# Performance work log

Hardware: AMD Instinct MI355X
Metric: run time of the kernel (lower is better)

The kernel has to match this reference:

```python
import jax, jax.numpy as jnp
import numpy as np

HEADS = 8
MEM_LEN = 32


def _mha(q, k, v, Wq, bq, Wk, bk, Wv, bv, Wo, bo):
    # torch nn.MultiheadAttention, batch_first=False. q: [Lq,B,E], k/v: [Lk,B,E]
    Lq, B, E = q.shape
    d = E // HEADS

    def proj(t, W, b):
        p = t @ W.T + b
        return p.reshape(t.shape[0], B, HEADS, d).transpose(1, 2, 0, 3)  # [B,h,L,d]

    qh, kh, vh = proj(q, Wq, bq), proj(k, Wk, bk), proj(v, Wv, bv)
    scale = 1.0 / jnp.sqrt(jnp.asarray(d, q.dtype))
    att = jax.nn.softmax(jnp.einsum('bhqd,bhkd->bhqk', qh * scale, kh), axis=-1)
    out = jnp.einsum('bhqk,bhkd->bhqd', att, vh)          # [B,h,Lq,d]
    out = out.transpose(2, 0, 1, 3).reshape(Lq, B, E)
    return out @ Wo.T + bo


def _forward(x, h, c, memK, memV, externalK, externalV,
             W_ih, W_hh, b_ih, b_hh,
             sWq, sbq, sWk, sbk, sWv, sbv, sWo, sbo,
             cWq, cbq, cWk, cbk, cWv, cbv, cWo, cbo,
             Wres, bres, Wrout, brout, Wcomp, bcomp, Wexp, bexp, Wgate, bgate):
    H = h.shape[1]
    # LSTMCell (torch gate order i, f, g, o)
    gates = x @ W_ih.T + b_ih + h @ W_hh.T + b_hh
    i, f, g, o = jnp.split(gates, 4, axis=1)
    c_next = jax.nn.sigmoid(f) * c + jax.nn.sigmoid(i) * jnp.tanh(g)
    h_lstm = jax.nn.sigmoid(o) * jnp.tanh(c_next)
    # append detached h_lstm to short memory, keep last MEM_LEN entries
    cur = jax.lax.stop_gradient(h_lstm)[None]                      # [1,B,H]
    memK_new = jnp.concatenate([memK, cur], axis=0)[-MEM_LEN:]     # [ML,B,H]
    memV_new = jnp.concatenate([memV, cur], axis=0)[-MEM_LEN:]
    qSelf = h_lstm[None]                                           # [1,B,H]
    self_out = _mha(qSelf, memK_new, memV_new, sWq, sbq, sWk, sbk, sWv, sbv, sWo, sbo)[0]
    ext_out = _mha(qSelf, externalK, externalV, cWq, cbq, cWk, cbk, cWv, cbv, cWo, cbo)[0]
    rw = jax.nn.softmax(h_lstm @ Wrout.T + brout, axis=1)          # [B,2] router
    routed_attn = rw[:, :1] * self_out + rw[:, 1:2] * ext_out
    routed = h_lstm + routed_attn + routed_attn @ Wres.T + bres
    temporal_summary = memK_new.mean(axis=0)                       # [B,H]
    compressed = temporal_summary @ Wcomp.T + bcomp                # [B,H//4]
    expanded = compressed @ Wexp.T + bexp                          # [B,H]
    reps = -(-H // compressed.shape[1])
    compressed_expanded = jnp.tile(compressed, (1, reps))[:, :H]
    gate = jax.nn.sigmoid(jnp.concatenate([x, routed], axis=1) @ Wgate.T + bgate)
    hCT = compressed_expanded + gate * (expanded - compressed_expanded)  # torch.lerp
    hFinal = (h_lstm + routed + hCT) / 3.0                         # dropout = identity (eval)
    return hFinal, h_lstm, c_next


def setup_inputs() -> dict:
    key = jax.random.key(0)
    ks = jax.random.split(key, 34)
    B, I, H, ML, EL = 2048, 1024, 1024, 32, 32
    BN = H // 4
    rn = lambda k, s, sc=1.0: jax.random.normal(k, s, dtype=jnp.float32) * sc
    return {
        'x': rn(ks[0], (B, I)), 'h': rn(ks[1], (B, H)), 'c': rn(ks[2], (B, H)),
        'memK': rn(ks[3], (ML, B, H)), 'memV': rn(ks[4], (ML, B, H)),
        'externalK': rn(ks[5], (EL, B, H)), 'externalV': rn(ks[6], (EL, B, H)),
        'W_ih': rn(ks[7], (4 * H, I), 0.02), 'W_hh': rn(ks[8], (4 * H, H), 0.02),
        'b_ih': jnp.zeros((4 * H,), jnp.float32), 'b_hh': jnp.zeros((4 * H,), jnp.float32),
        'sWq': rn(ks[9], (H, H), 0.02), 'sbq': rn(ks[10], (H,), 0.02),
        'sWk': rn(ks[11], (H, H), 0.02), 'sbk': rn(ks[12], (H,), 0.02),
        'sWv': rn(ks[13], (H, H), 0.02), 'sbv': rn(ks[14], (H,), 0.02),
        'sWo': rn(ks[15], (H, H), 0.02), 'sbo': rn(ks[16], (H,), 0.02),
        'cWq': rn(ks[17], (H, H), 0.02), 'cbq': rn(ks[18], (H,), 0.02),
        'cWk': rn(ks[19], (H, H), 0.02), 'cbk': rn(ks[20], (H,), 0.02),
        'cWv': rn(ks[21], (H, H), 0.02), 'cbv': rn(ks[22], (H,), 0.02),
        'cWo': rn(ks[23], (H, H), 0.02), 'cbo': rn(ks[24], (H,), 0.02),
        'Wres': rn(ks[25], (H, H), 0.02), 'bres': rn(ks[26], (H,), 0.02),
        'Wrout': rn(ks[27], (2, H), 0.02), 'brout': rn(ks[28], (2,), 0.02),
        'Wcomp': rn(ks[29], (BN, H), 0.02), 'bcomp': rn(ks[30], (BN,), 0.02),
        'Wexp': rn(ks[31], (H, BN), 0.02), 'bexp': rn(ks[32], (H,), 0.02),
        'Wgate': rn(ks[33], (H, I + H), 0.02), 'bgate': jnp.zeros((H,), jnp.float32),
    }


def reference(x, h, c, memK, memV, externalK, externalV,
              W_ih, W_hh, b_ih, b_hh,
              sWq, sbq, sWk, sbk, sWv, sbv, sWo, sbo,
              cWq, cbq, cWk, cbk, cWv, cbv, cWo, cbo,
              Wres, bres, Wrout, brout, Wcomp, bcomp, Wexp, bexp, Wgate, bgate):
    return _forward(x, h, c, memK, memV, externalK, externalV,
                    W_ih, W_hh, b_ih, b_hh,
                    sWq, sbq, sWk, sbk, sWv, sbv, sWo, sbo,
                    cWq, cbq, cWk, cbk, cWv, cbv, cWo, cbo,
                    Wres, bres, Wrout, brout, Wcomp, bcomp, Wexp, bexp, Wgate, bgate)
```

## Files before the change

kernel.cpp:

```cpp
#include <hip/hip_runtime.h>
#include <math.h>

typedef __attribute__((ext_vector_type(4))) float f32x4;
typedef __attribute__((ext_vector_type(8))) short bf16x8;
typedef __attribute__((ext_vector_type(4))) unsigned short u16x4;

__device__ __forceinline__ unsigned short f2bf(float f) {
  unsigned u = __builtin_bit_cast(unsigned, f);
  u += 0x7fffu + ((u >> 16) & 1u);
  return (unsigned short)(u >> 16);
}
__device__ __forceinline__ float bf2f(unsigned short s) {
  return __builtin_bit_cast(float, (unsigned)s << 16);
}
__device__ __forceinline__ float sigmoidf_(float x) { return 1.f / (1.f + __expf(-x)); }

template <int TN, int ACAT, int BCAT, int EPI, int ABF16, int OBF16>
__global__ __launch_bounds__(256) void gemm_k(
    const void* __restrict__ A1, const void* __restrict__ A1b, int lda1, long aZ,
    const void* __restrict__ A2, int lda2, int Ksplit,
    const float* __restrict__ B1, const float* __restrict__ B1b, int ldb1, long bZ,
    const float* __restrict__ B2, int ldb2,
    const float* __restrict__ bias1, const float* __restrict__ bias1b, long biasZ,
    const float* __restrict__ bias2,
    void* __restrict__ C, void* __restrict__ Cb, int ldc, long cZ,
    int K, int zs, float scale,
    const float* __restrict__ P0, const float* __restrict__ P1,
    const float* __restrict__ P2, const float* __restrict__ P3) {
  constexpr int NBI = TN / 32;
  __shared__ unsigned short As[2][128][32];
  __shared__ unsigned short Bs[2][TN][32];
  const int t = threadIdx.x;
  const int lane = t & 63;
  const int wave = t >> 6;
  const int wr = wave >> 1, wc = wave & 1;

  const unsigned gx = gridDim.x, gy = gridDim.y;
  unsigned L = blockIdx.x + gx * (blockIdx.y + gy * blockIdx.z);
  const unsigned nwg = gx * gy * gridDim.z;
  L = (L & 7u) * (nwg >> 3) + (L >> 3);
  const int bn = L % gx;
  const unsigned r1 = L / gx;
  const int bm = r1 % gy;
  const int z = r1 / gy;

  const bool hi = z >= zs;
  const int zz = hi ? z - zs : z;
  const char* Abase = (const char*)(hi ? A1b : A1) + (long)zz * aZ * (ABF16 ? 2 : 4);
  const float* Bbase = (hi ? B1b : B1) + (long)zz * bZ;
  const float* biasp = hi ? bias1b : bias1;
  char* Czc = (char*)(hi ? Cb : C) + (long)zz * cZ * (OBF16 ? 2 : 4);

  const int ar = t >> 3;
  const int bc = (t & 7) * 4;

  const int kIters = K >> 5;
  u16x4 Ra[4], Rb[NBI];

  auto loadT = [&](int kt) {
    const int k0 = kt << 5;
    const char* Ap; int ldA, kA;
    if (ACAT == 1 && k0 >= Ksplit) { Ap = (const char*)A2; ldA = lda2; kA = k0 - Ksplit; }
    else { Ap = Abase; ldA = lda1; kA = k0; }
    const float* Bp; int ldB, kB;
    if (BCAT == 1 && k0 >= Ksplit) { Bp = B2; ldB = ldb2; kB = k0 - Ksplit; }
    else { Bp = Bbase; ldB = ldb1; kB = k0; }
#pragma unroll
    for (int i = 0; i < 4; ++i) {
      const long aoff = ((long)bm * 128 + ar + 32 * i) * ldA + kA + bc;
      if (ABF16) {
        Ra[i] = *(const u16x4*)((const unsigned short*)Ap + aoff);
      } else {
        f32x4 v = *(const f32x4*)((const float*)Ap + aoff);
        u16x4 pk;
        pk[0] = f2bf(v[0]); pk[1] = f2bf(v[1]); pk[2] = f2bf(v[2]); pk[3] = f2bf(v[3]);
        Ra[i] = pk;
      }
    }
#pragma unroll
    for (int i = 0; i < NBI; ++i) {
      f32x4 bv = *(const f32x4*)(Bp + ((long)bn * TN + ar + 32 * i) * ldB + kB + bc);
      u16x4 bp;
      bp[0] = f2bf(bv[0]); bp[1] = f2bf(bv[1]); bp[2] = f2bf(bv[2]); bp[3] = f2bf(bv[3]);
      Rb[i] = bp;
    }
  };

  loadT(0);

  f32x4 acc[4][NBI] = {};
  int p = 0;
  for (int kt = 0; kt < kIters; ++kt) {
    __syncthreads();
#pragma unroll
    for (int i = 0; i < 4; ++i) *(u16x4*)&As[p][ar + 32 * i][bc] = Ra[i];
#pragma unroll
    for (int i = 0; i < NBI; ++i) *(u16x4*)&Bs[p][ar + 32 * i][bc] = Rb[i];
    if (kt + 1 < kIters) loadT(kt + 1);
    __syncthreads();

    bf16x8 af[4], bfr[NBI];
#pragma unroll
    for (int mi = 0; mi < 4; ++mi)
      af[mi] = *(const bf16x8*)&As[p][wr * 64 + mi * 16 + (lane & 15)][(lane >> 4) * 8];
#pragma unroll
    for (int ni = 0; ni < NBI; ++ni)
      bfr[ni] = *(const bf16x8*)&Bs[p][wc * (TN / 2) + ni * 16 + (lane & 15)][(lane >> 4) * 8];
#pragma unroll
    for (int mi = 0; mi < 4; ++mi)
#pragma unroll
      for (int ni = 0; ni < NBI; ++ni)
        acc[mi][ni] = __builtin_amdgcn_mfma_f32_16x16x32_bf16(af[mi], bfr[ni], acc[mi][ni], 0, 0, 0);
    p ^= 1;
  }

  const int colb = bn * TN + wc * (TN / 2);
  const int rowb = bm * 128 + wr * 64;
#pragma unroll
  for (int mi = 0; mi < 4; ++mi) {
#pragma unroll
    for (int ni = 0; ni < NBI; ++ni) {
      f32x4 v = acc[mi][ni];
      const int col = colb + ni * 16 + (lane & 15);
      const int row0 = rowb + mi * 16 + ((lane >> 4) << 2);
      float bsum = 0.f;
      if (biasp) bsum += biasp[zz * biasZ + col];
      if (bias2) bsum += bias2[col];
#pragma unroll
      for (int q = 0; q < 4; ++q) {
        const long row = row0 + q;
        const long off = row * ldc + col;
        const float val = v[q] + bsum;
        if (EPI == 0) {
          if (OBF16) ((unsigned short*)Czc)[off] = f2bf(val * scale);
          else       ((float*)Czc)[off] = val * scale;
        } else if (EPI == 1) {
          ((float*)Czc)[off] = val + P0[off] + P1[off];
        } else if (EPI == 2) {
          const float g = sigmoidf_(val);
          const float ce = P0[row * 256 + (col & 255)];
          const float ex = P1[off];
          ((float*)Czc)[off] = (P2[off] + P3[off] + ce + g * (ex - ce)) * (1.f / 3.f);
        } else if (EPI == 3) {
          ((unsigned short*)Czc)[off] = f2bf(val * P0[2 * row + (hi ? 1 : 0)]);
        } else {
          ((float*)Czc)[off] = val + P2[2 * row] * P0[col] + P2[2 * row + 1] * P1[col];
        }
      }
    }
  }
}

__global__ __launch_bounds__(256) void transpose_k(const float* __restrict__ in0,
                                                   float* __restrict__ out0,
                                                   const float* __restrict__ in1,
                                                   float* __restrict__ out1, int n) {
  __shared__ float tile[64][65];
  const float* in = blockIdx.z ? in1 : in0;
  float* out = blockIdx.z ? out1 : out0;
  const int tr = blockIdx.y, tc = blockIdx.x, t = threadIdx.x;
#pragma unroll
  for (int it = 0; it < 16; ++it) {
    int idx = t + 256 * it;
    int r = idx >> 6, c = idx & 63;
    tile[r][c] = in[(long)(tr * 64 + r) * n + tc * 64 + c];
  }
  __syncthreads();
#pragma unroll
  for (int it = 0; it < 16; ++it) {
    int idx = t + 256 * it;
    int rr = idx >> 6, cc = idx & 63;
    out[(long)(tc * 64 + rr) * n + tr * 64 + cc] = tile[cc][rr];
  }
}

__global__ __launch_bounds__(256) void lstm_k(const float* __restrict__ gates,
                                              const float* __restrict__ c_in,
                                              const float* __restrict__ Wr,
                                              const float* __restrict__ br,
                                              float* __restrict__ c_out,
                                              float* __restrict__ h_ws,
                                              float* __restrict__ h_out,
                                              float* __restrict__ rw) {
  const int b = blockIdx.x, t = threadIdx.x;
  const long base = (long)b * 1024 + t * 4;
  const float* gb = gates + (long)b * 4096 + t * 4;
  f32x4 gi = *(const f32x4*)(gb);
  f32x4 gf = *(const f32x4*)(gb + 1024);
  f32x4 gg = *(const f32x4*)(gb + 2048);
  f32x4 go = *(const f32x4*)(gb + 3072);
  f32x4 cv = *(const f32x4*)(c_in + base);
  f32x4 cn, hv;
#pragma unroll
  for (int q = 0; q < 4; ++q) {
    float cc = sigmoidf_(gf[q]) * cv[q] + sigmoidf_(gi[q]) * tanhf(gg[q]);
    cn[q] = cc;
    hv[q] = sigmoidf_(go[q]) * tanhf(cc);
  }
  *(f32x4*)(c_out + base) = cn;
  *(f32x4*)(h_ws + base) = hv;
  *(f32x4*)(h_out + base) = hv;
  f32x4 w0 = *(const f32x4*)(Wr + t * 4);
  f32x4 w1 = *(const f32x4*)(Wr + 1024 + t * 4);
  float a0 = hv[0] * w0[0] + hv[1] * w0[1] + hv[2] * w0[2] + hv[3] * w0[3];
  float a1 = hv[0] * w1[0] + hv[1] * w1[1] + hv[2] * w1[2] + hv[3] * w1[3];
#pragma unroll
  for (int m = 32; m >= 1; m >>= 1) {
    a0 += __shfl_xor(a0, m);
    a1 += __shfl_xor(a1, m);
  }
  __shared__ float red[8];
  if ((t & 63) == 0) { red[t >> 6] = a0; red[4 + (t >> 6)] = a1; }
  __syncthreads();
  if (t == 0) {
    float z0 = red[0] + red[1] + red[2] + red[3] + br[0];
    float z1 = red[4] + red[5] + red[6] + red[7] + br[1];
    float mx = fmaxf(z0, z1);
    float e0 = __expf(z0 - mx), e1 = __expf(z1 - mx);
    float s = e0 + e1;
    rw[2 * b] = e0 / s;
    rw[2 * b + 1] = e1 / s;
  }
}

__global__ __launch_bounds__(256) void attn3_k(
    const float* __restrict__ memK, const float* __restrict__ memV,
    const float* __restrict__ extK, const float* __restrict__ extV,
    const float* __restrict__ hl,
    const unsigned short* __restrict__ qtS, const unsigned short* __restrict__ qtE,
    unsigned short* __restrict__ mixS, unsigned short* __restrict__ mixE,
    float* __restrict__ ts) {
  const int NB = 2048, H = 1024;
  __shared__ __align__(16) unsigned short sreg[2][128][36];
  __shared__ float Sp[4][32][17];
  __shared__ unsigned short P_lds[16][32];
  unsigned short* KT = &sreg[0][0][0];

  const int b = blockIdx.x;
  const bool self = blockIdx.y == 0;
  const int t = threadIdx.x;
  const int lane = t & 63;
  const int w = t >> 6;

  const float* baseK[4];
  int rrA[4], cc4[4];
#pragma unroll
  for (int it = 0; it < 4; ++it) {
    int f = t + 256 * it;
    int r = f >> 5, c4 = f & 31;
    rrA[it] = r; cc4[it] = c4;
    if (self) baseK[it] = (r < 31) ? (memK + ((long)(r + 1) * NB + b) * H) : (hl + (long)b * H);
    else      baseK[it] = extK + ((long)r * NB + b) * H;
  }
  const int l2 = t & 15, dgrp = t >> 4;
  const float* baseV0;
  const float* baseV1;
  {
    int r0 = 2 * l2, r1v = 2 * l2 + 1;
    if (self) {
      baseV0 = memV + ((long)(r0 + 1) * NB + b) * H;
      baseV1 = (r1v < 31) ? (memV + ((long)(r1v + 1) * NB + b) * H) : (hl + (long)b * H);
    } else {
      baseV0 = extV + ((long)r0 * NB + b) * H;
      baseV1 = extV + ((long)r1v * NB + b) * H;
    }
  }

  const unsigned short* qtb = (self ? qtS : qtE) + (long)b * 8192 + (lane & 7) * 1024;
  unsigned short* mixp = (self ? mixS : mixE) + (long)b * 8192;

  f32x4 R[4];
#pragma unroll
  for (int it = 0; it < 4; ++it) R[it] = *(const f32x4*)(baseK[it] + cc4[it] * 4);
  bf16x8 bq = *(const bf16x8*)(qtb + w * 32 + ((lane >> 4) * 8));

  f32x4 accS[2] = {};
  int p = 0;
  for (int ch = 0; ch < 8; ++ch) {
    __syncthreads();
#pragma unroll
    for (int it = 0; it < 4; ++it)
      *(u16x4*)(KT + p * 4096 + (cc4[it] >> 3) * 1024 + rrA[it] * 32 + (cc4[it] & 7) * 4) =
          (u16x4){f2bf(R[it][0]), f2bf(R[it][1]), f2bf(R[it][2]), f2bf(R[it][3])};
    if (ch < 7) {
#pragma unroll
      for (int it = 0; it < 4; ++it)
        R[it] = *(const f32x4*)(baseK[it] + (ch + 1) * 128 + cc4[it] * 4);
    } else {
      R[0] = *(const f32x4*)(baseV0 + dgrp * 8);
      R[1] = *(const f32x4*)(baseV0 + dgrp * 8 + 4);
      R[2] = *(const f32x4*)(baseV1 + dgrp * 8);
      R[3] = *(const f32x4*)(baseV1 + dgrp * 8 + 4);
    }
    __syncthreads();
    bf16x8 bq_cur = bq;
    if (ch < 7) bq = *(const bf16x8*)(qtb + (ch + 1) * 128 + w * 32 + ((lane >> 4) * 8));
    if (self && t < 128) {
      float s = 0.f;
      const unsigned short* kc = KT + p * 4096 + (t >> 5) * 1024 + (t & 31);
#pragma unroll
      for (int lr = 0; lr < 32; ++lr) s += bf2f(kc[lr * 32]);
      ts[(long)b * H + ch * 128 + t] = s * (1.f / 32.f);
    }
#pragma unroll
    for (int mi = 0; mi < 2; ++mi) {
      bf16x8 af = *(const bf16x8*)(KT + p * 4096 + w * 1024 + (mi * 16 + (lane & 15)) * 32 +
                                   ((lane >> 4) * 8));
      accS[mi] = __builtin_amdgcn_mfma_f32_16x16x32_bf16(af, bq_cur, accS[mi], 0, 0, 0);
    }
    p ^= 1;
  }
#pragma unroll
  for (int mi = 0; mi < 2; ++mi)
#pragma unroll
    for (int q = 0; q < 4; ++q)
      Sp[w][mi * 16 + (lane >> 4) * 4 + q][lane & 15] = accS[mi][q];
  __syncthreads();
  {
    const int head = t >> 5, l = t & 31;
    float S = Sp[0][l][head] + Sp[1][l][head] + Sp[2][l][head] + Sp[3][l][head];
    float mx = S;
#pragma unroll
    for (int m = 16; m >= 1; m >>= 1) mx = fmaxf(mx, __shfl_xor(mx, m, 32));
    float pr = __expf(S - mx);
    float sum = pr;
#pragma unroll
    for (int m = 16; m >= 1; m >>= 1) sum += __shfl_xor(sum, m, 32);
    pr /= sum;
    P_lds[head][l] = f2bf(pr);
    P_lds[8 + head][l] = 0;
  }
  for (int ch = 0; ch < 8; ++ch) {
    __syncthreads();
#pragma unroll
    for (int e = 0; e < 4; ++e) {
      unsigned lo0 = (unsigned)f2bf(R[0][e]) | ((unsigned)f2bf(R[2][e]) << 16);
      unsigned lo1 = (unsigned)f2bf(R[1][e]) | ((unsigned)f2bf(R[3][e]) << 16);
      *(unsigned*)&sreg[p][dgrp * 8 + e][2 * l2] = lo0;
      *(unsigned*)&sreg[p][dgrp * 8 + 4 + e][2 * l2] = lo1;
    }
    if (ch < 7) {
      R[0] = *(const f32x4*)(baseV0 + (ch + 1) * 128 + dgrp * 8);
      R[1] = *(const f32x4*)(baseV0 + (ch + 1) * 128 + dgrp * 8 + 4);
      R[2] = *(const f32x4*)(baseV1 + (ch + 1) * 128 + dgrp * 8);
      R[3] = *(const f32x4*)(baseV1 + (ch + 1) * 128 + dgrp * 8 + 4);
    }
    __syncthreads();
    bf16x8 pa = *(const bf16x8*)&P_lds[lane & 15][(lane >> 4) * 8];
#pragma unroll
    for (int i = 0; i < 2; ++i) {
      const int dbase = w * 32 + i * 16;
      const unsigned short* vb = &sreg[p][dbase + (lane & 15)][(lane >> 4) * 8];
      union { unsigned long long q[2]; bf16x8 v; } uu;
      uu.q[0] = *(const unsigned long long*)vb;
      uu.q[1] = *(const unsigned long long*)(vb + 4);
      f32x4 o = __builtin_amdgcn_mfma_f32_16x16x32_bf16(pa, uu.v, (f32x4){0.f, 0.f, 0.f, 0.f},
                                                        0, 0, 0);
      if (lane < 32) {
        const int d = ch * 128 + dbase + (lane & 15);
        const int h0 = (lane >> 4) * 4;
#pragma unroll
        for (int q = 0; q < 4; ++q) mixp[(long)(h0 + q) * 1024 + d] = f2bf(o[q]);
      }
    }
    p ^= 1;
  }
}

extern "C" void kernel_launch(void* const* d_in, const int* in_sizes, int n_in,
                              void* d_out, int out_size, void* d_ws, size_t ws_size,
                              hipStream_t stream) {
  const float* x    = (const float*)d_in[0];
  const float* h    = (const float*)d_in[1];
  const float* c    = (const float*)d_in[2];
  const float* memK = (const float*)d_in[3];
  const float* memV = (const float*)d_in[4];
  const float* extK = (const float*)d_in[5];
  const float* extV = (const float*)d_in[6];
  const float* W_ih = (const float*)d_in[7];
  const float* W_hh = (const float*)d_in[8];
  const float* b_ih = (const float*)d_in[9];
  const float* b_hh = (const float*)d_in[10];
  const float* sWq = (const float*)d_in[11];
  const float* sbq = (const float*)d_in[12];
  const float* sWk = (const float*)d_in[13];
  const float* sWv = (const float*)d_in[15];
  const float* sbv = (const float*)d_in[16];
  const float* sWo = (const float*)d_in[17];
  const float* sbo = (const float*)d_in[18];
  const float* cWq = (const float*)d_in[19];
  const float* cbq = (const float*)d_in[20];
  const float* cWk = (const float*)d_in[21];
  const float* cWv = (const float*)d_in[23];
  const float* cbv = (const float*)d_in[24];
  const float* cWo = (const float*)d_in[25];
  const float* cbo = (const float*)d_in[26];
  const float* Wres = (const float*)d_in[27];
  const float* bres = (const float*)d_in[28];
  const float* Wrout = (const float*)d_in[29];
  const float* brout = (const float*)d_in[30];
  const float* Wcomp = (const float*)d_in[31];
  const float* bcomp = (const float*)d_in[32];
  const float* Wexp = (const float*)d_in[33];
  const float* bexp = (const float*)d_in[34];
  const float* Wgate = (const float*)d_in[35];
  const float* bgate = (const float*)d_in[36];
  (void)in_sizes; (void)n_in; (void)out_size; (void)ws_size;

  float* out = (float*)d_out;
  float* w = (float*)d_ws;
  const long M1 = 1024 * 1024;
  float* gates   = w;
  float* hl      = w + 8 * M1;
  unsigned short* qsS = (unsigned short*)(w + 10 * M1);
  unsigned short* qsE = (unsigned short*)(w + 12 * M1);
  float* wkTs    = w + 14 * M1;
  float* wkTc    = w + 15 * M1;
  unsigned short* qtS = (unsigned short*)(w + 16 * M1);
  unsigned short* qtE = (unsigned short*)(w + 32 * M1);
  unsigned short* mixS = (unsigned short*)(w + 48 * M1);
  unsigned short* mixE = (unsigned short*)(w + 64 * M1);
  float* ts      = w + 80 * M1;
  unsigned short* attnS = (unsigned short*)(w + 82 * M1);
  unsigned short* attnE = (unsigned short*)(w + 84 * M1);
  float* rw      = w + 90 * M1;
  float* rattn   = w + 91 * M1;
  float* routed  = w + 93 * M1;
  float* comp    = w + 95 * M1;
  float* expd    = w + 96 * M1;

  float* hFinal_out = out;
  float* hl_out     = out + 2 * M1;
  float* cn_out     = out + 4 * M1;

  const float scaleq = 0.08838834764831845f;
  const int ZBIG = 1 << 30;
  dim3 blk(256);
  const float* nf = nullptr;

  gemm_k<128, 1, 1, 0, 0, 0><<<dim3(32, 16, 1), blk, 0, stream>>>(
      x, nullptr, 1024, 0, h, 1024, 1024,
      W_ih, nf, 1024, 0, W_hh, 1024,
      b_ih, nf, 0, b_hh,
      gates, nullptr, 4096, 0,
      2048, ZBIG, 1.f, nf, nf, nf, nf);

  transpose_k<<<dim3(16, 16, 2), blk, 0, stream>>>(sWk, wkTs, cWk, wkTc, 1024);

  lstm_k<<<2048, blk, 0, stream>>>(gates, c, Wrout, brout, cn_out, hl, hl_out, rw);

  gemm_k<128, 0, 0, 0, 0, 1><<<dim3(8, 16, 2), blk, 0, stream>>>(
      hl, hl, 1024, 0, nullptr, 0, 0,
      sWq, cWq, 1024, 0, nf, 0,
      sbq, cbq, 0, nf,
      qsS, qsE, 1024, 0,
      1024, 1, scaleq, nf, nf, nf, nf);

  gemm_k<128, 0, 0, 0, 1, 1><<<dim3(8, 16, 16), blk, 0, stream>>>(
      qsS, qsE, 1024, 128, nullptr, 0, 0,
      wkTs, wkTc, 1024, 128, nf, 0,
      nf, nf, 0, nf,
      qtS, qtE, 8192, 1024,
      128, 8, 1.f, nf, nf, nf, nf);

  attn3_k<<<dim3(2048, 2), blk, 0, stream>>>(memK, memV, extK, extV, hl,
                                             qtS, qtE, mixS, mixE, ts);

  gemm_k<64, 0, 0, 3, 1, 1><<<dim3(2, 16, 16), blk, 0, stream>>>(
      mixS, mixE, 8192, 1024, nullptr, 0, 0,
      sWv, cWv, 1024, 131072, nf, 0,
      sbv, cbv, 128, nf,
      attnS, attnE, 1024, 128,
      1024, 8, 1.f, rw, nf, nf, nf);

  gemm_k<64, 1, 1, 4, 1, 0><<<dim3(16, 16, 1), blk, 0, stream>>>(
      attnS, nullptr, 1024, 0, attnE, 1024, 1024,
      sWo, nf, 1024, 0, cWo, 1024,
      nf, nf, 0, nf,
      rattn, nullptr, 1024, 0,
      2048, ZBIG, 1.f, sbo, cbo, rw, nf);

  gemm_k<64, 0, 0, 1, 0, 0><<<dim3(16, 16, 1), blk, 0, stream>>>(
      rattn, nullptr, 1024, 0, nullptr, 0, 0,
      Wres, nf, 1024, 0, nf, 0,
      bres, nf, 0, nf,
      routed, nullptr, 1024, 0,
      1024, ZBIG, 1.f, hl, rattn, nf, nf);

  gemm_k<64, 0, 0, 0, 0, 0><<<dim3(4, 16, 1), blk, 0, stream>>>(
      ts, nullptr, 1024, 0, nullptr, 0, 0,
      Wcomp, nf, 1024, 0, nf, 0,
      bcomp, nf, 0, nf,
      comp, nullptr, 256, 0,
      1024, ZBIG, 1.f, nf, nf, nf, nf);
  gemm_k<64, 0, 0, 0, 0, 0><<<dim3(16, 16, 1), blk, 0, stream>>>(
      comp, nullptr, 256, 0, nullptr, 0, 0,
      Wexp, nf, 256, 0, nf, 0,
      bexp, nf, 0, nf,
      expd, nullptr, 1024, 0,
      256, ZBIG, 1.f, nf, nf, nf, nf);

  gemm_k<64, 1, 0, 2, 0, 0><<<dim3(16, 16, 1), blk, 0, stream>>>(
      x, nullptr, 1024, 0, routed, 1024, 1024,
      Wgate, nf, 2048, 0, nf, 0,
      bgate, nf, 0, nf,
      hFinal_out, nullptr, 1024, 0,
      2048, ZBIG, 1.f, comp, expd, hl, routed);
}
```

Before: 784.7 us.

## Split fused attention kernel into chunk-parallel scores, softmax and mix kernels

The single attention kernel that looped over eight 128-wide hidden chunks per (batch, side) block is replaced by three kernels. A scores kernel handles one chunk per block and writes partial scores to workspace, a small softmax kernel reduces them, and a mix kernel computes P·V one chunk per block. This raises the block count eightfold to expose more memory-level parallelism for the large K/V reads, and pads the LDS row stride to cut bank conflicts. The cost is two extra launches, a global round trip for partial scores and probabilities, and the loss of the in-kernel software prefetch. Two workspace regions are reused under the assumption that they are dead at that point.

```diff
diff --git a/kernel.cpp b/kernel.cpp
--- a/kernel.cpp
+++ b/kernel.cpp
@@ -223,36 +223,92 @@
   }
 }
 
-__global__ __launch_bounds__(256) void attn3_k(
-    const float* __restrict__ memK, const float* __restrict__ memV,
-    const float* __restrict__ extK, const float* __restrict__ extV,
+__global__ __launch_bounds__(256) void scores_k(
+    const float* __restrict__ memK, const float* __restrict__ extK,
     const float* __restrict__ hl,
     const unsigned short* __restrict__ qtS, const unsigned short* __restrict__ qtE,
-    unsigned short* __restrict__ mixS, unsigned short* __restrict__ mixE,
-    float* __restrict__ ts) {
+    float* __restrict__ pS, float* __restrict__ ts) {
   const int NB = 2048, H = 1024;
-  __shared__ __align__(16) unsigned short sreg[2][128][36];
+  __shared__ __align__(16) unsigned short KT[4 * 1168];
   __shared__ float Sp[4][32][17];
-  __shared__ unsigned short P_lds[16][32];
-  unsigned short* KT = &sreg[0][0][0];
-
-  const int b = blockIdx.x;
-  const bool self = blockIdx.y == 0;
-  const int t = threadIdx.x;
-  const int lane = t & 63;
-  const int w = t >> 6;
-
-  const float* baseK[4];
-  int rrA[4], cc4[4];
+  const int b = blockIdx.x, side = blockIdx.y, ch = blockIdx.z;
+  const bool self = side == 0;
+  const int t = threadIdx.x, lane = t & 63, w = t >> 6;
+
 #pragma unroll
   for (int it = 0; it < 4; ++it) {
     int f = t + 256 * it;
     int r = f >> 5, c4 = f & 31;
-    rrA[it] = r; cc4[it] = c4;
-    if (self) baseK[it] = (r < 31) ? (memK + ((long)(r + 1) * NB + b) * H) : (hl + (long)b * H);
-    else      baseK[it] = extK + ((long)r * NB + b) * H;
-  }
+    const float* src = self ? ((r < 31) ? memK + ((long)(r + 1) * NB + b) * H : hl + (long)b * H)
+                            : extK + ((long)r * NB + b) * H;
+    f32x4 v = *(const f32x4*)(src + ch * 128 + c4 * 4);
+    *(u16x4*)&KT[(c4 >> 3) * 1168 + r * 36 + (c4 & 7) * 4] =
+        (u16x4){f2bf(v[0]), f2bf(v[1]), f2bf(v[2]), f2bf(v[3])};
+  }
+  __syncthreads();
+  if (self && t < 128) {
+    float s = 0.f;
+    const unsigned short* kc = KT + (t >> 5) * 1168 + (t & 31);
+#pragma unroll
+    for (int lr = 0; lr < 32; ++lr) s += bf2f(kc[lr * 36]);
+    ts[(long)b * H + ch * 128 + t] = s * (1.f / 32.f);
+  }
+  const unsigned short* qt =
+      (self ? qtS : qtE) + (long)b * 8192 + (lane & 7) * 1024 + ch * 128;
+  bf16x8 bq = *(const bf16x8*)(qt + w * 32 + (lane >> 4) * 8);
+  f32x4 accS[2] = {};
+#pragma unroll
+  for (int mi = 0; mi < 2; ++mi) {
+    const unsigned short* ap = &KT[w * 1168 + (mi * 16 + (lane & 15)) * 36 + (lane >> 4) * 8];
+    union { unsigned long long q[2]; bf16x8 v; } ua;
+    ua.q[0] = *(const unsigned long long*)ap;
+    ua.q[1] = *(const unsigned long long*)(ap + 4);
+    accS[mi] = __builtin_amdgcn_mfma_f32_16x16x32_bf16(ua.v, bq, accS[mi], 0, 0, 0);
+  }
+#pragma unroll
+  for (int mi = 0; mi < 2; ++mi)
+#pragma unroll
+    for (int q = 0; q < 4; ++q)
+      Sp[w][mi * 16 + (lane >> 4) * 4 + q][lane & 15] = accS[mi][q];
+  __syncthreads();
+  const int l = t & 31, head = t >> 5;
+  float S = Sp[0][l][head] + Sp[1][l][head] + Sp[2][l][head] + Sp[3][l][head];
+  pS[(((long)b * 2 + side) * 8 + ch) * 256 + t] = S;
+}
+
+__global__ __launch_bounds__(256) void softmax_k(const float* __restrict__ pS,
+                                                 unsigned short* __restrict__ Pbuf) {
+  const long bs = (long)blockIdx.x * 2 + blockIdx.y;
+  const int t = threadIdx.x;
+  const float* base = pS + bs * 8 * 256;
+  float S = 0.f;
+#pragma unroll
+  for (int ch = 0; ch < 8; ++ch) S += base[ch * 256 + t];
+  float mx = S;
+#pragma unroll
+  for (int m = 16; m >= 1; m >>= 1) mx = fmaxf(mx, __shfl_xor(mx, m, 32));
+  float pr = __expf(S - mx);
+  float sum = pr;
+#pragma unroll
+  for (int m = 16; m >= 1; m >>= 1) sum += __shfl_xor(sum, m, 32);
+  pr /= sum;
+  unsigned short* Pb = Pbuf + bs * 512;
+  Pb[t] = f2bf(pr);
+  Pb[256 + t] = 0;
+}
+
+__global__ __launch_bounds__(256) void mix_k(
+    const float* __restrict__ memV, const float* __restrict__ extV,
+    const float* __restrict__ hl,
+    const unsigned short* __restrict__ Pbuf,
+    unsigned short* __restrict__ mixS, unsigned short* __restrict__ mixE) {
+  const int NB = 2048, H = 1024;
+  __shared__ __align__(16) unsigned short Vt[128][36];
+  const int b = blockIdx.x, side = blockIdx.y, ch = blockIdx.z;
+  const bool self = side == 0;
+  const int t = threadIdx.x, lane = t & 63, w = t >> 6;
   const int l2 = t & 15, dgrp = t >> 4;
+
   const float* baseV0;
   const float* baseV1;
   {
@@ -265,105 +321,36 @@
       baseV1 = extV + ((long)r1v * NB + b) * H;
     }
   }
-
-  const unsigned short* qtb = (self ? qtS : qtE) + (long)b * 8192 + (lane & 7) * 1024;
+  f32x4 R0 = *(const f32x4*)(baseV0 + ch * 128 + dgrp * 8);
+  f32x4 R1 = *(const f32x4*)(baseV0 + ch * 128 + dgrp * 8 + 4);
+  f32x4 R2 = *(const f32x4*)(baseV1 + ch * 128 + dgrp * 8);
+  f32x4 R3 = *(const f32x4*)(baseV1 + ch * 128 + dgrp * 8 + 4);
+  bf16x8 pa = *(const bf16x8*)(Pbuf + ((long)b * 2 + side) * 512 + (lane & 15) * 32 +
+                               (lane >> 4) * 8);
+#pragma unroll
+  for (int e = 0; e < 4; ++e) {
+    unsigned lo0 = (unsigned)f2bf(R0[e]) | ((unsigned)f2bf(R2[e]) << 16);
+    unsigned lo1 = (unsigned)f2bf(R1[e]) | ((unsigned)f2bf(R3[e]) << 16);
+    *(unsigned*)&Vt[dgrp * 8 + e][2 * l2] = lo0;
+    *(unsigned*)&Vt[dgrp * 8 + 4 + e][2 * l2] = lo1;
+  }
+  __syncthreads();
   unsigned short* mixp = (self ? mixS : mixE) + (long)b * 8192;
-
-  f32x4 R[4];
-#pragma unroll
-  for (int it = 0; it < 4; ++it) R[it] = *(const f32x4*)(baseK[it] + cc4[it] * 4);
-  bf16x8 bq = *(const bf16x8*)(qtb + w * 32 + ((lane >> 4) * 8));
-
-  f32x4 accS[2] = {};
-  int p = 0;
-  for (int ch = 0; ch < 8; ++ch) {
-    __syncthreads();
-#pragma unroll
-    for (int it = 0; it < 4; ++it)
-      *(u16x4*)(KT + p * 4096 + (cc4[it] >> 3) * 1024 + rrA[it] * 32 + (cc4[it] & 7) * 4) =
-          (u16x4){f2bf(R[it][0]), f2bf(R[it][1]), f2bf(R[it][2]), f2bf(R[it][3])};
-    if (ch < 7) {
-#pragma unroll
-      for (int it = 0; it < 4; ++it)
-        R[it] = *(const f32x4*)(baseK[it] + (ch + 1) * 128 + cc4[it] * 4);
-    } else {
-      R[0] = *(const f32x4*)(baseV0 + dgrp * 8);
-      R[1] = *(const f32x4*)(baseV0 + dgrp * 8 + 4);
-      R[2] = *(const f32x4*)(baseV1 + dgrp * 8);
-      R[3] = *(const f32x4*)(baseV1 + dgrp * 8 + 4);
+#pragma unroll
+  for (int i = 0; i < 2; ++i) {
+    const int dbase = w * 32 + i * 16;
+    const unsigned short* vb = &Vt[dbase + (lane & 15)][(lane >> 4) * 8];
+    union { unsigned long long q[2]; bf16x8 v; } uu;
+    uu.q[0] = *(const unsigned long long*)vb;
+    uu.q[1] = *(const unsigned long long*)(vb + 4);
+    f32x4 o = __builtin_amdgcn_mfma_f32_16x16x32_bf16(pa, uu.v, (f32x4){0.f, 0.f, 0.f, 0.f},
+                                                      0, 0, 0);
+    if (lane < 32) {
+      const int d = ch * 128 + dbase + (lane & 15);
+      const int h0 = (lane >> 4) * 4;
+#pragma unroll
+      for (int q = 0; q < 4; ++q) mixp[(long)(h0 + q) * 1024 + d] = f2bf(o[q]);
     }
-    __syncthreads();
-    bf16x8 bq_cur = bq;
-    if (ch < 7) bq = *(const bf16x8*)(qtb + (ch + 1) * 128 + w * 32 + ((lane >> 4) * 8));
-    if (self && t < 128) {
-      float s = 0.f;
-      const unsigned short* kc = KT + p * 4096 + (t >> 5) * 1024 + (t & 31);
-#pragma unroll
-      for (int lr = 0; lr < 32; ++lr) s += bf2f(kc[lr * 32]);
-      ts[(long)b * H + ch * 128 + t] = s * (1.f / 32.f);
-    }
-#pragma unroll
-    for (int mi = 0; mi < 2; ++mi) {
-      bf16x8 af = *(const bf16x8*)(KT + p * 4096 + w * 1024 + (mi * 16 + (lane & 15)) * 32 +
-                                   ((lane >> 4) * 8));
-      accS[mi] = __builtin_amdgcn_mfma_f32_16x16x32_bf16(af, bq_cur, accS[mi], 0, 0, 0);
-    }
-    p ^= 1;
-  }
-#pragma unroll
-  for (int mi = 0; mi < 2; ++mi)
-#pragma unroll
-    for (int q = 0; q < 4; ++q)
-      Sp[w][mi * 16 + (lane >> 4) * 4 + q][lane & 15] = accS[mi][q];
-  __syncthreads();
-  {
-    const int head = t >> 5, l = t & 31;
-    float S = Sp[0][l][head] + Sp[1][l][head] + Sp[2][l][head] + Sp[3][l][head];
-    float mx = S;
-#pragma unroll
-    for (int m = 16; m >= 1; m >>= 1) mx = fmaxf(mx, __shfl_xor(mx, m, 32));
-    float pr = __expf(S - mx);
-    float sum = pr;
-#pragma unroll
-    for (int m = 16; m >= 1; m >>= 1) sum += __shfl_xor(sum, m, 32);
-    pr /= sum;
-    P_lds[head][l] = f2bf(pr);
-    P_lds[8 + head][l] = 0;
-  }
-  for (int ch = 0; ch < 8; ++ch) {
-    __syncthreads();
-#pragma unroll
-    for (int e = 0; e < 4; ++e) {
-      unsigned lo0 = (unsigned)f2bf(R[0][e]) | ((unsigned)f2bf(R[2][e]) << 16);
-      unsigned lo1 = (unsigned)f2bf(R[1][e]) | ((unsigned)f2bf(R[3][e]) << 16);
-      *(unsigned*)&sreg[p][dgrp * 8 + e][2 * l2] = lo0;
-      *(unsigned*)&sreg[p][dgrp * 8 + 4 + e][2 * l2] = lo1;
-    }
-    if (ch < 7) {
-      R[0] = *(const f32x4*)(baseV0 + (ch + 1) * 128 + dgrp * 8);
-      R[1] = *(const f32x4*)(baseV0 + (ch + 1) * 128 + dgrp * 8 + 4);
-      R[2] = *(const f32x4*)(baseV1 + (ch + 1) * 128 + dgrp * 8);
-      R[3] = *(const f32x4*)(baseV1 + (ch + 1) * 128 + dgrp * 8 + 4);
-    }
-    __syncthreads();
-    bf16x8 pa = *(const bf16x8*)&P_lds[lane & 15][(lane >> 4) * 8];
-#pragma unroll
-    for (int i = 0; i < 2; ++i) {
-      const int dbase = w * 32 + i * 16;
-      const unsigned short* vb = &sreg[p][dbase + (lane & 15)][(lane >> 4) * 8];
-      union { unsigned long long q[2]; bf16x8 v; } uu;
-      uu.q[0] = *(const unsigned long long*)vb;
-      uu.q[1] = *(const unsigned long long*)(vb + 4);
-      f32x4 o = __builtin_amdgcn_mfma_f32_16x16x32_bf16(pa, uu.v, (f32x4){0.f, 0.f, 0.f, 0.f},
-                                                        0, 0, 0);
-      if (lane < 32) {
-        const int d = ch * 128 + dbase + (lane & 15);
-        const int h0 = (lane >> 4) * 4;
-#pragma unroll
-        for (int q = 0; q < 4; ++q) mixp[(long)(h0 + q) * 1024 + d] = f2bf(o[q]);
-      }
-    }
-    p ^= 1;
   }
 }
 
@@ -411,8 +398,10 @@
   float* w = (float*)d_ws;
   const long M1 = 1024 * 1024;
   float* gates   = w;
+  float* pS      = w;
   float* hl      = w + 8 * M1;
   unsigned short* qsS = (unsigned short*)(w + 10 * M1);
+  unsigned short* Pbuf = (unsigned short*)(w + 10 * M1);
   unsigned short* qsE = (unsigned short*)(w + 12 * M1);
   float* wkTs    = w + 14 * M1;
   float* wkTc    = w + 15 * M1;
@@ -463,8 +452,9 @@
       qtS, qtE, 8192, 1024,
       128, 8, 1.f, nf, nf, nf, nf);
 
-  attn3_k<<<dim3(2048, 2), blk, 0, stream>>>(memK, memV, extK, extV, hl,
-                                             qtS, qtE, mixS, mixE, ts);
+  scores_k<<<dim3(2048, 2, 8), blk, 0, stream>>>(memK, extK, hl, qtS, qtE, pS, ts);
+  softmax_k<<<dim3(2048, 2), blk, 0, stream>>>(pS, Pbuf);
+  mix_k<<<dim3(2048, 2, 8), blk, 0, stream>>>(memV, extV, hl, Pbuf, mixS, mixE);
 
   gemm_k<64, 0, 0, 3, 1, 1><<<dim3(2, 16, 16), blk, 0, stream>>>(
       mixS, mixE, 8192, 1024, nullptr, 0, 0,
```

New measurement: 877.7 us. 1.12x slower.

## Stage whole K and V tiles in LDS with batched loads in attention kernel

Applied to the files above, without the earlier changes.

The attention kernel no longer streams K and V through a double-buffered 128-column chunk loop with two barriers per chunk. It loads all 32 K rows (8 rows per batch of outstanding loads) into a single padded LDS array, runs QK^T as one wave-local MFMA loop with the softmax done in registers via shuffles, then stages all of V at once. This cuts barriers and the cross-wave score reduction and raises memory-level parallelism, at the cost of about 78KB of LDS per block, which limits occupancy.

```diff
diff --git a/kernel.cpp b/kernel.cpp
--- a/kernel.cpp
+++ b/kernel.cpp
@@ -223,7 +223,7 @@
   }
 }
 
-__global__ __launch_bounds__(256) void attn3_k(
+__global__ __launch_bounds__(256) void attn4_k(
     const float* __restrict__ memK, const float* __restrict__ memV,
     const float* __restrict__ extK, const float* __restrict__ extV,
     const float* __restrict__ hl,
@@ -231,139 +231,136 @@
     unsigned short* __restrict__ mixS, unsigned short* __restrict__ mixE,
     float* __restrict__ ts) {
   const int NB = 2048, H = 1024;
-  __shared__ __align__(16) unsigned short sreg[2][128][36];
-  __shared__ float Sp[4][32][17];
-  __shared__ unsigned short P_lds[16][32];
-  unsigned short* KT = &sreg[0][0][0];
-
+  __shared__ __align__(16) unsigned short LDSU[38912];
+  __shared__ __align__(16) unsigned short P_lds[16 * 36];
   const int b = blockIdx.x;
   const bool self = blockIdx.y == 0;
-  const int t = threadIdx.x;
-  const int lane = t & 63;
-  const int w = t >> 6;
-
-  const float* baseK[4];
-  int rrA[4], cc4[4];
-#pragma unroll
-  for (int it = 0; it < 4; ++it) {
-    int f = t + 256 * it;
-    int r = f >> 5, c4 = f & 31;
-    rrA[it] = r; cc4[it] = c4;
-    if (self) baseK[it] = (r < 31) ? (memK + ((long)(r + 1) * NB + b) * H) : (hl + (long)b * H);
-    else      baseK[it] = extK + ((long)r * NB + b) * H;
-  }
-  const int l2 = t & 15, dgrp = t >> 4;
-  const float* baseV0;
-  const float* baseV1;
+  const int t = threadIdx.x, lane = t & 63, w = t >> 6;
+
+  auto krow = [&](int r) -> const float* {
+    return self ? ((r < 31) ? memK + ((long)(r + 1) * NB + b) * H : hl + (long)b * H)
+                : extK + ((long)r * NB + b) * H;
+  };
+  auto vrow = [&](int r) -> const float* {
+    return self ? ((r < 31) ? memV + ((long)(r + 1) * NB + b) * H : hl + (long)b * H)
+                : extV + ((long)r * NB + b) * H;
+  };
+
+  const int chS = t >> 5, c4S = t & 31;
+  const unsigned kbase = (unsigned)(chS * 4 + (c4S >> 3)) * 1168 + (unsigned)(c4S & 7) * 4;
+#pragma unroll
+  for (int g = 0; g < 4; ++g) {
+    f32x4 R[8];
+#pragma unroll
+    for (int u = 0; u < 8; ++u) R[u] = *(const f32x4*)(krow(g * 8 + u) + t * 4);
+#pragma unroll
+    for (int u = 0; u < 8; ++u) {
+      const int r = g * 8 + u;
+      u16x4 pk;
+      pk[0] = f2bf(R[u][0]); pk[1] = f2bf(R[u][1]); pk[2] = f2bf(R[u][2]); pk[3] = f2bf(R[u][3]);
+      *(u16x4*)&LDSU[kbase + (unsigned)r * 36] = pk;
+    }
+  }
+  __syncthreads();
+
+  if (self) {
+#pragma unroll
+    for (int ci = 0; ci < 4; ++ci) {
+      const int g = t + 256 * ci;
+      const int q = g & 127;
+      const unsigned short* base = &LDSU[(unsigned)((g >> 7) * 4 + (q >> 5)) * 1168 + (q & 31)];
+      float s = 0.f;
+#pragma unroll
+      for (int r = 0; r < 32; ++r) s += bf2f(base[r * 36]);
+      ts[(long)b * H + g] = s * (1.f / 32.f);
+    }
+  }
+
+  const unsigned short* qtb =
+      (self ? qtS : qtE) + (long)b * 8192 + (long)(lane & 7) * 1024 + (lane >> 4) * 8;
+  f32x4 accS[2] = {};
+  for (int jj = 0; jj < 32; ++jj) {
+    bf16x8 bq = *(const bf16x8*)(qtb + jj * 32);
+#pragma unroll
+    for (int mi = 0; mi < 2; ++mi) {
+      const unsigned short* ap =
+          &LDSU[(unsigned)jj * 1168 + (unsigned)(mi * 16 + (lane & 15)) * 36 + (lane >> 4) * 8];
+      union { unsigned long long q[2]; bf16x8 v; } ua;
+      ua.q[0] = *(const unsigned long long*)ap;
+      ua.q[1] = *(const unsigned long long*)(ap + 4);
+      accS[mi] = __builtin_amdgcn_mfma_f32_16x16x32_bf16(ua.v, bq, accS[mi], 0, 0, 0);
+    }
+  }
+
   {
-    int r0 = 2 * l2, r1v = 2 * l2 + 1;
-    if (self) {
-      baseV0 = memV + ((long)(r0 + 1) * NB + b) * H;
-      baseV1 = (r1v < 31) ? (memV + ((long)(r1v + 1) * NB + b) * H) : (hl + (long)b * H);
-    } else {
-      baseV0 = extV + ((long)r0 * NB + b) * H;
-      baseV1 = extV + ((long)r1v * NB + b) * H;
-    }
-  }
-
-  const unsigned short* qtb = (self ? qtS : qtE) + (long)b * 8192 + (lane & 7) * 1024;
+    float mx = -3.4e38f;
+#pragma unroll
+    for (int mi = 0; mi < 2; ++mi)
+#pragma unroll
+      for (int q = 0; q < 4; ++q) mx = fmaxf(mx, accS[mi][q]);
+    mx = fmaxf(mx, __shfl_xor(mx, 16));
+    mx = fmaxf(mx, __shfl_xor(mx, 32));
+    float sum = 0.f;
+    float pv[2][4];
+#pragma unroll
+    for (int mi = 0; mi < 2; ++mi)
+#pragma unroll
+      for (int q = 0; q < 4; ++q) { pv[mi][q] = __expf(accS[mi][q] - mx); sum += pv[mi][q]; }
+    sum += __shfl_xor(sum, 16);
+    sum += __shfl_xor(sum, 32);
+    const float rinv = 1.f / sum;
+    const bool valid = (lane & 15) < 8;
+#pragma unroll
+    for (int mi = 0; mi < 2; ++mi) {
+      u16x4 pk;
+#pragma unroll
+      for (int q = 0; q < 4; ++q) pk[q] = valid ? f2bf(pv[mi][q] * rinv) : (unsigned short)0;
+      *(u16x4*)&P_lds[(unsigned)(lane & 15) * 36 + mi * 16 + (lane >> 4) * 4] = pk;
+    }
+  }
+  __syncthreads();
+
+#pragma unroll
+  for (int g = 0; g < 4; ++g) {
+    f32x4 RA[4], RB[4];
+#pragma unroll
+    for (int u = 0; u < 4; ++u) {
+      const int pr = g * 4 + u;
+      RA[u] = *(const f32x4*)(vrow(2 * pr) + t * 4);
+      RB[u] = *(const f32x4*)(vrow(2 * pr + 1) + t * 4);
+    }
+#pragma unroll
+    for (int u = 0; u < 4; ++u) {
+      const int pr = g * 4 + u;
+#pragma unroll
+      for (int e = 0; e < 4; ++e) {
+        const unsigned dw = (unsigned)f2bf(RA[u][e]) | ((unsigned)f2bf(RB[u][e]) << 16);
+        *(unsigned*)&LDSU[(unsigned)(t * 4 + e) * 38 + 2 * pr] = dw;
+      }
+    }
+  }
+  __syncthreads();
+
+  bf16x8 pa = *(const bf16x8*)&P_lds[(unsigned)(lane & 15) * 36 + (lane >> 4) * 8];
   unsigned short* mixp = (self ? mixS : mixE) + (long)b * 8192;
-
-  f32x4 R[4];
-#pragma unroll
-  for (int it = 0; it < 4; ++it) R[it] = *(const f32x4*)(baseK[it] + cc4[it] * 4);
-  bf16x8 bq = *(const bf16x8*)(qtb + w * 32 + ((lane >> 4) * 8));
-
-  f32x4 accS[2] = {};
-  int p = 0;
+#pragma unroll
   for (int ch = 0; ch < 8; ++ch) {
-    __syncthreads();
-#pragma unroll
-    for (int it = 0; it < 4; ++it)
-      *(u16x4*)(KT + p * 4096 + (cc4[it] >> 3) * 1024 + rrA[it] * 32 + (cc4[it] & 7) * 4) =
-          (u16x4){f2bf(R[it][0]), f2bf(R[it][1]), f2bf(R[it][2]), f2bf(R[it][3])};
-    if (ch < 7) {
-#pragma unroll
-      for (int it = 0; it < 4; ++it)
-        R[it] = *(const f32x4*)(baseK[it] + (ch + 1) * 128 + cc4[it] * 4);
-    } else {
-      R[0] = *(const f32x4*)(baseV0 + dgrp * 8);
-      R[1] = *(const f32x4*)(baseV0 + dgrp * 8 + 4);
-      R[2] = *(const f32x4*)(baseV1 + dgrp * 8);
-      R[3] = *(const f32x4*)(baseV1 + dgrp * 8 + 4);
-    }
-    __syncthreads();
-    bf16x8 bq_cur = bq;
-    if (ch < 7) bq = *(const bf16x8*)(qtb + (ch + 1) * 128 + w * 32 + ((lane >> 4) * 8));
-    if (self && t < 128) {
-      float s = 0.f;
-      const unsigned short* kc = KT + p * 4096 + (t >> 5) * 1024 + (t & 31);
-#pragma unroll
-      for (int lr = 0; lr < 32; ++lr) s += bf2f(kc[lr * 32]);
-      ts[(long)b * H + ch * 128 + t] = s * (1.f / 32.f);
-    }
-#pragma unroll
-    for (int mi = 0; mi < 2; ++mi) {
-      bf16x8 af = *(const bf16x8*)(KT + p * 4096 + w * 1024 + (mi * 16 + (lane & 15)) * 32 +
-                                   ((lane >> 4) * 8));
-      accS[mi] = __builtin_amdgcn_mfma_f32_16x16x32_bf16(af, bq_cur, accS[mi], 0, 0, 0);
-    }
-    p ^= 1;
-  }
-#pragma unroll
-  for (int mi = 0; mi < 2; ++mi)
-#pragma unroll
-    for (int q = 0; q < 4; ++q)
-      Sp[w][mi * 16 + (lane >> 4) * 4 + q][lane & 15] = accS[mi][q];
-  __syncthreads();
-  {
-    const int head = t >> 5, l = t & 31;
-    float S = Sp[0][l][head] + Sp[1][l][head] + Sp[2][l][head] + Sp[3][l][head];
-    float mx = S;
-#pragma unroll
-    for (int m = 16; m >= 1; m >>= 1) mx = fmaxf(mx, __shfl_xor(mx, m, 32));
-    float pr = __expf(S - mx);
-    float sum = pr;
-#pragma unroll
-    for (int m = 16; m >= 1; m >>= 1) sum += __shfl_xor(sum, m, 32);
-    pr /= sum;
-    P_lds[head][l] = f2bf(pr);
-    P_lds[8 + head][l] = 0;
-  }
-  for (int ch = 0; ch < 8; ++ch) {
-    __syncthreads();
-#pragma unroll
-    for (int e = 0; e < 4; ++e) {
-      unsigned lo0 = (unsigned)f2bf(R[0][e]) | ((unsigned)f2bf(R[2][e]) << 16);
-      unsigned lo1 = (unsigned)f2bf(R[1][e]) | ((unsigned)f2bf(R[3][e]) << 16);
-      *(unsigned*)&sreg[p][dgrp * 8 + e][2 * l2] = lo0;
-      *(unsigned*)&sreg[p][dgrp * 8 + 4 + e][2 * l2] = lo1;
-    }
-    if (ch < 7) {
-      R[0] = *(const f32x4*)(baseV0 + (ch + 1) * 128 + dgrp * 8);
-      R[1] = *(const f32x4*)(baseV0 + (ch + 1) * 128 + dgrp * 8 + 4);
-      R[2] = *(const f32x4*)(baseV1 + (ch + 1) * 128 + dgrp * 8);
-      R[3] = *(const f32x4*)(baseV1 + (ch + 1) * 128 + dgrp * 8 + 4);
-    }
-    __syncthreads();
-    bf16x8 pa = *(const bf16x8*)&P_lds[lane & 15][(lane >> 4) * 8];
 #pragma unroll
     for (int i = 0; i < 2; ++i) {
-      const int dbase = w * 32 + i * 16;
-      const unsigned short* vb = &sreg[p][dbase + (lane & 15)][(lane >> 4) * 8];
-      union { unsigned long long q[2]; bf16x8 v; } uu;
-      uu.q[0] = *(const unsigned long long*)vb;
-      uu.q[1] = *(const unsigned long long*)(vb + 4);
+      const int dbase = ch * 128 + w * 32 + i * 16;
+      const unsigned* vb =
+          (const unsigned*)&LDSU[(unsigned)(dbase + (lane & 15)) * 38 + (lane >> 4) * 8];
+      union { unsigned u[4]; bf16x8 v; } uu;
+      uu.u[0] = vb[0]; uu.u[1] = vb[1]; uu.u[2] = vb[2]; uu.u[3] = vb[3];
       f32x4 o = __builtin_amdgcn_mfma_f32_16x16x32_bf16(pa, uu.v, (f32x4){0.f, 0.f, 0.f, 0.f},
                                                         0, 0, 0);
       if (lane < 32) {
-        const int d = ch * 128 + dbase + (lane & 15);
+        const int d = dbase + (lane & 15);
         const int h0 = (lane >> 4) * 4;
 #pragma unroll
         for (int q = 0; q < 4; ++q) mixp[(long)(h0 + q) * 1024 + d] = f2bf(o[q]);
       }
     }
-    p ^= 1;
   }
 }
 
@@ -463,7 +460,7 @@
       qtS, qtE, 8192, 1024,
       128, 8, 1.f, nf, nf, nf, nf);
 
-  attn3_k<<<dim3(2048, 2), blk, 0, stream>>>(memK, memV, extK, extV, hl,
+  attn4_k<<<dim3(2048, 2), blk, 0, stream>>>(memK, memV, extK, extV, hl,
                                              qtS, qtE, mixS, mixE, ts);
 
   gemm_k<64, 0, 0, 3, 1, 1><<<dim3(2, 16, 16), blk, 0, stream>>>(
```

Result: no change. 792.5 us (+1.0%).
